# Kernel optimization log

Hardware: AMD Instinct MI355X
Metric: run time of the kernel (lower is better)

The kernel has to match this reference:

```python
import jax, jax.numpy as jnp
import numpy as np

EPS = 1e-6
NUM_CHANNELS = 8


def rotate_half(x):
    h = x.shape[-1] // 2
    return jnp.concatenate([-x[..., h:], x[..., :h]], axis=-1)


def l1_normalize(x):
    # torch F.normalize(p=1): x / max(||x||_1, eps) along last dim
    n = jnp.sum(jnp.abs(x), axis=-1, keepdims=True)
    return x / jnp.maximum(n, EPS)


def squared_softmax(x):      # potential_func_z = 'square'
    return l1_normalize(x * x)


def abs_normalization(x):    # potential_func_g = 'abs'
    return l1_normalize(jax.nn.relu(x))


def head_selection(qz, u, v, cos, sin):
    b, s, d = qz.shape
    C = NUM_CHANNELS
    r = u.shape[0] // C
    cos_e = cos[:, None]  # [b,1,s,r] (unsqueeze_dim=1)
    sin_e = sin[:, None]
    ap = lambda x: x * cos_e + rotate_half(x) * sin_e
    ap_o = lambda x: x * cos_e - rotate_half(x) * sin_e
    # [b,s,C*r] -> [b,C,s,r]
    qz_u = (qz @ u.T).reshape(b, s, C, r).transpose(0, 2, 1, 3)
    qz_v = (qz @ v.T).reshape(b, s, C, r).transpose(0, 2, 1, 3)
    qz_uo = ap_o(qz_u)
    qz_u = ap(qz_u)
    qz_v = ap(qz_v)
    msg_F = jnp.einsum('bcqr,bckr->bcqk', qz_u, qz_v)          # [b,C,s,s]
    # regularize_h = 1/dim_z -> softmax(F * dim_z)
    qh = jax.nn.softmax(msg_F.astype(jnp.float32) * d, axis=-1).astype(qz_u.dtype)
    qh_v1 = jnp.einsum('bcqk,bckr->bcqr', qh, qz_v)
    qh_v2 = jnp.einsum('bcqk,bcqr->bckr', qh, qz_uo)           # qh^T @ qz_uo
    qh_v1 = ap_o(qh_v1).transpose(0, 2, 1, 3).reshape(b, s, C * r)
    qh_v2 = ap(qh_v2).transpose(0, 2, 1, 3).reshape(b, s, C * r)
    return qh_v1 @ u + qh_v2 @ v                               # ternary_factor_scaling = 1


def topic_modeling(qz, w):
    qg = abs_normalization(qz @ w.T)     # binary_factor_scaling = regularize_g = 1
    return qg @ w


def period_message(qz, period_mat, period_attn):
    # info = P @ qz @ A, single term since _lambda = 0
    return jnp.einsum('qk,bkd->bqd', period_mat, qz) @ period_attn


def reference(unary, cos, sin, ternary_u, ternary_v, binary_factor,
              period_mat, period_attn, num_iters):
    # mean-field iterator: qz = act_z((unary + messages)/regularize_z), regularize_z = 1
    qz = squared_softmax(unary)
    for _ in range(num_iters):
        msg = (head_selection(qz, ternary_u, ternary_v, cos, sin)
               + topic_modeling(qz, binary_factor)
               + period_message(qz, period_mat, period_attn))
        qz = squared_softmax(unary + msg)
    return qz


def setup_inputs() -> dict:
    key = jax.random.key(0)
    ks = jax.random.split(key, 4)
    b, s, d, dff = 2, 2048, 256, 1024
    C = NUM_CHANNELS
    r = d // C  # head_dim = 32
    unary = jax.random.normal(ks[0], (b, s, d), dtype=jnp.float32)
    # RoPE tables (theta = 10000)
    inv_freq = 1.0 / (10000.0 ** (np.arange(0, r, 2, dtype=np.float32) / r))
    pos = np.arange(s, dtype=np.float32)
    freqs = pos[:, None] * inv_freq[None, :]
    emb = np.concatenate([freqs, freqs], axis=-1)               # [s, r]
    cos = jnp.broadcast_to(jnp.asarray(np.cos(emb))[None], (b, s, r)).astype(jnp.float32)
    sin = jnp.broadcast_to(jnp.asarray(np.sin(emb))[None], (b, s, r)).astype(jnp.float32)
    std = 0.2
    ternary_u = jax.random.normal(ks[1], (C * r, d), dtype=jnp.float32) * std
    ternary_v = jax.random.normal(ks[2], (C * r, d), dtype=jnp.float32) * std
    binary_factor = jax.random.normal(ks[3], (dff, d), dtype=jnp.float32) * std
    # PTPeriod buffers: band |i-j| == 24, and decaying matrix (k=1 -> identity)
    i = np.arange(s)
    period_mat = jnp.asarray((np.abs(i[:, None] - i[None, :]) == 24).astype(np.float32))
    j = np.arange(d)
    dist = np.abs(j[:, None] - j[None, :]).astype(np.float32)
    attn = np.exp(-0.5 * dist ** 2)
    attn[dist >= 1.0] = 0.0
    period_attn = jnp.asarray(attn, dtype=jnp.float32)
    return {"unary": unary, "cos": cos, "sin": sin,
            "ternary_u": ternary_u, "ternary_v": ternary_v,
            "binary_factor": binary_factor,
            "period_mat": period_mat, "period_attn": period_attn,
            "num_iters": 3}
```

## Files before the change

### kernel.cpp

```cpp
#include <hip/hip_runtime.h>
#include <math.h>

#define B 2
#define S 2048
#define D 256
#define DFF 1024
#define NC 8
#define R 32
#define NITER 3
#define EPSV 1e-6f
#define MROW (B * S)
#define NSPLIT 4

typedef unsigned short u16;
typedef unsigned int u32;
typedef __attribute__((ext_vector_type(8))) short short8_t;
typedef __attribute__((ext_vector_type(4))) float f32x4;

#define MFMA16(a, b, c) __builtin_amdgcn_mfma_f32_16x16x32_bf16(a, b, c, 0, 0, 0)

__device__ inline u16 bf16_rne(float x) {
  u32 u = __float_as_uint(x);
  u32 r = u + 0x7FFFu + ((u >> 16) & 1u);
  return (u16)(r >> 16);
}
__device__ inline void split2(float x, u16& h, u16& l) {
  h = bf16_rne(x);
  float hf = __uint_as_float(((u32)h) << 16);
  l = bf16_rne(x - hf);
}
__device__ inline short8_t ld8(const u16* p) { return *(const short8_t*)p; }

__device__ inline u32 pk2(float a, float b) {
  u32 r;
  asm("v_cvt_pk_bf16_f32 %0, %1, %2" : "=v"(r) : "v"(a), "v"(b));
  return r;
}
__device__ inline short8_t pack8(float c0, float c1, float c2, float c3,
                                 float c4, float c5, float c6, float c7) {
  union { u32 w[4]; short8_t v; } u_;
  u_.w[0] = pk2(c0, c1);
  u_.w[1] = pk2(c2, c3);
  u_.w[2] = pk2(c4, c5);
  u_.w[3] = pk2(c6, c7);
  return u_.v;
}

__device__ inline void gload_lds16(const u16* g, u16* l) {
  __builtin_amdgcn_global_load_lds(
      (const __attribute__((address_space(1))) unsigned int*)g,
      (__attribute__((address_space(3))) unsigned int*)l, 16, 0, 0);
}

__global__ __launch_bounds__(256) void k_sqsm(const float* __restrict__ unary,
                                              const float* __restrict__ msgs,
                                              const float* __restrict__ qzp,
                                              const int* __restrict__ pcols,
                                              const float* __restrict__ pvals,
                                              const int* __restrict__ pcnt,
                                              float* __restrict__ outf,
                                              u16* __restrict__ qzz) {
  int row = blockIdx.x;
  int t = threadIdx.x;
  int i = row * D + t;
  float x = unary[i];
  if (msgs) {
    const size_t NEl = (size_t)MROW * D;
#pragma unroll
    for (int p = 0; p < NSPLIT; p++) x += msgs[p * NEl + i];
    int b = row >> 11, q = row & 2047;
    int n = pcnt[q];
    for (int j = 0; j < n; j++)
      x = fmaf(pvals[q * 16 + j], qzp[(size_t)(b * S + pcols[q * 16 + j]) * D + t], x);
  }
  float v = x * x;
  float s = v;
#pragma unroll
  for (int off = 32; off; off >>= 1) s += __shfl_down(s, off, 64);
  __shared__ float red[4];
  if ((t & 63) == 0) red[t >> 6] = s;
  __syncthreads();
  float tot = fmaxf(red[0] + red[1] + red[2] + red[3], EPSV);
  float y = v / tot;
  if (outf) outf[i] = y;
  u16 h, l;
  split2(y, h, l);
  size_t rb = (size_t)row * 512;
  qzz[rb + t] = h;
  qzz[rb + 256 + t] = l;
}

__global__ __launch_bounds__(256) void k_gemm_z(
    const u16* __restrict__ Az, const u16* __restrict__ Bz,
    int K2, int Kpart, int N,
    float* __restrict__ outbase,
    float* __restrict__ quv, float* __restrict__ qg, float* __restrict__ qzp) {
  int Kh = K2 / 3;
  int Alda = Kh * 2;
  int m0 = blockIdx.x * 128, n0 = blockIdx.y * 128;
  int kbeg = blockIdx.z * Kpart, kend = kbeg + Kpart;
  int tid = threadIdx.x;
  int wid = tid >> 6, lane = tid & 63;
  int lr = lane & 15, lg = lane >> 4;
  int wm = (wid >> 1) * 64, wn = (wid & 1) * 64;

  __shared__ alignas(16) u16 As[8192];
  __shared__ alignas(16) u16 Bs[8192];

  f32x4 acc[4][4];
#pragma unroll
  for (int fr = 0; fr < 4; fr++)
#pragma unroll
    for (int fc = 0; fc < 4; fc++) acc[fr][fc] = (f32x4){0.f, 0.f, 0.f, 0.f};

  for (int kk = kbeg; kk < kend; kk += 64) {
    int zsrc = (kk >= Kh) ? kk - Kh : kk;
    __syncthreads();
#pragma unroll
    for (int it = 0; it < 4; it++) {
      int f = (it * 256 + tid) * 16;
      int row = f >> 7;
      int c16 = ((f >> 4) & 7) ^ (row & 7);
      u16* ldst = (u16*)As + it * 2048 + wid * 512;
      gload_lds16(Az + (size_t)(m0 + row) * Alda + zsrc + c16 * 8, ldst);
      u16* ldstB = (u16*)Bs + it * 2048 + wid * 512;
      gload_lds16(Bz + (size_t)(n0 + row) * K2 + kk + c16 * 8, ldstB);
    }
    __syncthreads();
#pragma unroll
    for (int ks = 0; ks < 2; ks++) {
      int cb = ks * 4 + lg;
      int sw = (cb ^ (lr & 7)) << 3;
      short8_t af[4], bf[4];
#pragma unroll
      for (int fr = 0; fr < 4; fr++)
        af[fr] = *(const short8_t*)(As + ((wm + fr * 16 + lr) << 6) + sw);
#pragma unroll
      for (int fc = 0; fc < 4; fc++)
        bf[fc] = *(const short8_t*)(Bs + ((wn + fc * 16 + lr) << 6) + sw);
      __builtin_amdgcn_s_setprio(1);
#pragma unroll
      for (int fr = 0; fr < 4; fr++)
#pragma unroll
        for (int fc = 0; fc < 4; fc++)
          acc[fr][fc] = MFMA16(af[fr], bf[fc], acc[fr][fc]);
      __builtin_amdgcn_s_setprio(0);
    }
  }

  if (qg) {
#pragma unroll
    for (int fr = 0; fr < 4; fr++)
#pragma unroll
      for (int fc = 0; fc < 4; fc++)
#pragma unroll
        for (int i = 0; i < 4; i++) {
          int m = m0 + wm + fr * 16 + lg * 4 + i;
          int nn = n0 + wn + fc * 16 + lr;
          float x = acc[fr][fc][i];
          if (nn < 512) quv[(size_t)m * 512 + nn] = x;
          else if (nn < 1536) qg[(size_t)m * DFF + nn - 512] = fmaxf(x, 0.f);
          else qzp[(size_t)m * 256 + nn - 1536] = x;
        }
  } else {
    float* out = outbase + (size_t)blockIdx.z * ((size_t)gridDim.x * 128) * N;
#pragma unroll
    for (int fr = 0; fr < 4; fr++)
#pragma unroll
      for (int fc = 0; fc < 4; fc++)
#pragma unroll
        for (int i = 0; i < 4; i++) {
          int m = m0 + wm + fr * 16 + lg * 4 + i;
          int nn = n0 + wn + fc * 16 + lr;
          out[(size_t)m * N + nn] = acc[fr][fc][i];
        }
  }
}

__global__ __launch_bounds__(256) void k_rope_pre(
    const float* __restrict__ quv, const float* __restrict__ cosb,
    const float* __restrict__ sinb,
    u16* __restrict__ Ah, u16* __restrict__ Al,
    u16* __restrict__ Bvh, u16* __restrict__ Bvl,
    u16* __restrict__ BvTph, u16* __restrict__ AoTph) {
  int row = blockIdx.x;
  int b = row >> 11, s_ = row & 2047;
  int t = threadIdx.x, c = t >> 5, rr = t & 31;
  float qu = quv[(size_t)row * 512 + t];
  float qv = quv[(size_t)row * 512 + 256 + t];
  float ou = __shfl_xor(qu, 16, 64);
  float ov = __shfl_xor(qv, 16, 64);
  float ru = (rr < 16) ? -ou : ou;
  float rv = (rr < 16) ? -ov : ov;
  float cs = cosb[(size_t)(b * S + s_) * R + rr];
  float sn = sinb[(size_t)(b * S + s_) * R + rr];
  float a = (qu * cs + ru * sn) * 256.f;
  float ao = qu * cs - ru * sn;
  float bv = qv * cs + rv * sn;
  size_t o = ((size_t)(b * NC + c) * S + s_) * R + rr;
  int off = s_ & 63;
  int kt = off >> 4;
  int pp = (kt >> 1) * 32 + ((off >> 2) & 3) * 8 + (kt & 1) * 4 + (off & 3);
  size_t otp = ((size_t)(b * NC + c) * R + rr) * S + (size_t)((s_ & ~63) + pp);
  u16 h, l;
  split2(a, h, l);  Ah[o] = h;  Al[o] = l;
  split2(bv, h, l); Bvh[o] = h; Bvl[o] = l; BvTph[otp] = h;
  split2(ao, h, l); AoTph[otp] = h;
}

__global__ __launch_bounds__(1024) void k_attn1_mfma(
    const u16* __restrict__ Ah, const u16* __restrict__ Al,
    const u16* __restrict__ Bvh, const u16* __restrict__ Bvl,
    const u16* __restrict__ BvTph,
    float* __restrict__ O1, float* __restrict__ mbuf, float* __restrict__ lbuf) {
  int bidx = blockIdx.x;
  int xcd = bidx & 7, wv = bidx >> 3;
  int bc = xcd * 2 + (wv & 1);
  int tile = wv >> 1;
  int tid = threadIdx.x;
  int lane = tid & 63;
  int lr = lane & 15, lg = lane >> 4;
  int khs = tid >> 9;
  int w8 = (tid >> 6) & 7;
  int qr = tile * 128 + w8 * 16;
  const size_t ofs = (size_t)bc * S * R;
  const size_t ofsT = (size_t)bc * R * S;

  __shared__ alignas(16) u16 BvhS[2][2][2048];
  __shared__ alignas(16) u16 BvlS[2][2][2048];
  __shared__ alignas(16) u16 PvS[2][2][2048];
  __shared__ float cm_o[8][16][34];
  __shared__ float cm_m[8][16], cm_l[8][16];

  short8_t a_hi = ld8(Ah + ofs + (size_t)(qr + lr) * R + lg * 8);
  short8_t a_lo = ld8(Al + ofs + (size_t)(qr + lr) * R + lg * 8);

  f32x4 o0 = {0, 0, 0, 0}, o1 = {0, 0, 0, 0};
  float m_q = -1e30f, l_p = 0.f;

  int ci = (w8 & 3) * 64 + lane;
  int wql = (w8 & 3) * 512;

#define A1_STAGE(STEP, DB)                                                         \
  {                                                                                \
    int kb_ = khs * 1024 + (STEP) * 64;                                            \
    if (w8 < 4) {                                                                  \
      gload_lds16(Bvh + ofs + (size_t)(kb_ + (ci >> 2)) * R + (ci & 3) * 8,        \
                  &BvhS[DB][khs][wql]);                                            \
      gload_lds16(BvTph + ofsT + (size_t)(ci >> 3) * S + kb_ + (ci & 7) * 8,       \
                  &PvS[DB][khs][wql]);                                             \
    } else {                                                                       \
      gload_lds16(Bvl + ofs + (size_t)(kb_ + (ci >> 2)) * R + (ci & 3) * 8,        \
                  &BvlS[DB][khs][wql]);                                            \
    }                                                                              \
  }

  A1_STAGE(0, 0);
  for (int step = 0; step < 16; step++) {
    int db = step & 1;
    __syncthreads();
    if (step + 1 < 16) A1_STAGE(step + 1, db ^ 1);

    short8_t sbH[4], sbL[4], pvb[4];
#pragma unroll
    for (int kt = 0; kt < 4; kt++) {
      int ro = (kt * 16 + lr) * 32 + lg * 8;
      sbH[kt] = ld8(&BvhS[db][khs][ro]);
      sbL[kt] = ld8(&BvlS[db][khs][ro]);
    }
#pragma unroll
    for (int j = 0; j < 4; j++)
      pvb[j] = ld8(&PvS[db][khs][((j & 1) * 16 + lr) * 64 + (j >> 1) * 32 + lg * 8]);

    f32x4 c[4];
    __builtin_amdgcn_s_setprio(1);
#pragma unroll
    for (int kt = 0; kt < 4; kt++) {
      f32x4 cc = {0.f, 0.f, 0.f, 0.f};
      cc = MFMA16(sbH[kt], a_hi, cc);
      cc = MFMA16(sbH[kt], a_lo, cc);
      cc = MFMA16(sbL[kt], a_hi, cc);
      c[kt] = cc;
    }
    __builtin_amdgcn_s_setprio(0);
    float mx = -1e30f;
#pragma unroll
    for (int kt = 0; kt < 4; kt++)
#pragma unroll
      for (int i = 0; i < 4; i++) mx = fmaxf(mx, c[kt][i]);
    if (!__all((int)(mx <= m_q + 8.f))) {
      mx = fmaxf(mx, __shfl_xor(mx, 16, 64));
      mx = fmaxf(mx, __shfl_xor(mx, 32, 64));
      float mnew = fmaxf(m_q, mx);
      float sc = __expf(m_q - mnew);
      m_q = mnew;
      l_p *= sc;
#pragma unroll
      for (int i = 0; i < 4; i++) {
        float s4 = __shfl(sc, (lane & 48) | (lg * 4 + i), 64);
        o0[i] *= s4;
        o1[i] *= s4;
      }
    }
    float ps = 0.f;
#pragma unroll
    for (int kt = 0; kt < 4; kt++)
#pragma unroll
      for (int i = 0; i < 4; i++) {
        c[kt][i] = __expf(c[kt][i] - m_q);
        ps += c[kt][i];
      }
    l_p += ps;
    __builtin_amdgcn_s_setprio(1);
    short8_t f0h = pack8(c[0][0], c[0][1], c[0][2], c[0][3],
                         c[1][0], c[1][1], c[1][2], c[1][3]);
    short8_t f1h = pack8(c[2][0], c[2][1], c[2][2], c[2][3],
                         c[3][0], c[3][1], c[3][2], c[3][3]);
    o0 = MFMA16(f0h, pvb[0], o0);
    o1 = MFMA16(f0h, pvb[1], o1);
    o0 = MFMA16(f1h, pvb[2], o0);
    o1 = MFMA16(f1h, pvb[3], o1);
    __builtin_amdgcn_s_setprio(0);
  }

  float lq = l_p;
  lq += __shfl_xor(lq, 16, 64);
  lq += __shfl_xor(lq, 32, 64);
  float m4[4], l4[4];
#pragma unroll
  for (int i = 0; i < 4; i++) {
    int src = (lane & 48) | (lg * 4 + i);
    m4[i] = __shfl(m_q, src, 64);
    l4[i] = __shfl(lq, src, 64);
  }
  __syncthreads();
  if (khs == 1) {
#pragma unroll
    for (int i = 0; i < 4; i++) {
      int r_ = lg * 4 + i;
      cm_o[w8][r_][lr] = o0[i];
      cm_o[w8][r_][lr + 16] = o1[i];
      if (lr == 0) { cm_m[w8][r_] = m4[i]; cm_l[w8][r_] = l4[i]; }
    }
  }
  __syncthreads();
  if (khs == 0) {
#pragma unroll
    for (int i = 0; i < 4; i++) {
      int r_ = lg * 4 + i;
      int q = qr + r_;
      float mb = cm_m[w8][r_], lb = cm_l[w8][r_];
      float mN = fmaxf(m4[i], mb);
      float ea = __expf(m4[i] - mN), eb = __expf(mb - mN);
      float inv = 1.f / (l4[i] * ea + lb * eb);
      O1[ofs + (size_t)q * R + lr] = (o0[i] * ea + cm_o[w8][r_][lr] * eb) * inv;
      O1[ofs + (size_t)q * R + 16 + lr] = (o1[i] * ea + cm_o[w8][r_][lr + 16] * eb) * inv;
      if (lr == 0) {
        mbuf[(size_t)bc * S + q] = mN;
        lbuf[(size_t)bc * S + q] = inv;
      }
    }
  }
}

__global__ __launch_bounds__(1024) void k_attn2_mfma(
    const u16* __restrict__ Ah, const u16* __restrict__ Al,
    const u16* __restrict__ Bvh, const u16* __restrict__ Bvl,
    const u16* __restrict__ AoTph,
    const float* __restrict__ mbuf, const float* __restrict__ lbuf,
    float* __restrict__ O2) {
  int bidx = blockIdx.x;
  int xcd = bidx & 7, wv = bidx >> 3;
  int bc = xcd * 2 + (wv & 1);
  int tile = wv >> 1;
  int tid = threadIdx.x;
  int lane = tid & 63;
  int lr = lane & 15, lg = lane >> 4;
  int qhs = tid >> 9;
  int w8 = (tid >> 6) & 7;
  int kr = tile * 128 + w8 * 16;
  const size_t ofs = (size_t)bc * S * R;
  const size_t ofsT = (size_t)bc * R * S;

  __shared__ alignas(16) u16 AhS[2][2][2048];
  __shared__ alignas(16) u16 AlS[2][2][2048];
  __shared__ alignas(16) u16 PvS[2][2][2048];
  __shared__ float cm[8][16][34];

  short8_t bv_hi = ld8(Bvh + ofs + (size_t)(kr + lr) * R + lg * 8);
  short8_t bv_lo = ld8(Bvl + ofs + (size_t)(kr + lr) * R + lg * 8);

  f32x4 o0 = {0, 0, 0, 0}, o1 = {0, 0, 0, 0};

  int ci = (w8 & 3) * 64 + lane;
  int wql = (w8 & 3) * 512;

#define A2_STAGE(STEP, DB)                                                         \
  {                                                                                \
    int qb_ = qhs * 1024 + (STEP) * 64;                                            \
    if (w8 < 4) {                                                                  \
      gload_lds16(Ah + ofs + (size_t)(qb_ + (ci >> 2)) * R + (ci & 3) * 8,         \
                  &AhS[DB][qhs][wql]);                                             \
      gload_lds16(AoTph + ofsT + (size_t)(ci >> 3) * S + qb_ + (ci & 7) * 8,       \
                  &PvS[DB][qhs][wql]);                                             \
    } else {                                                                       \
      gload_lds16(Al + ofs + (size_t)(qb_ + (ci >> 2)) * R + (ci & 3) * 8,         \
                  &AlS[DB][qhs][wql]);                                             \
    }                                                                              \
  }

  A2_STAGE(0, 0);
  for (int step = 0; step < 16; step++) {
    int db = step & 1;
    __syncthreads();
    if (step + 1 < 16) A2_STAGE(step + 1, db ^ 1);

    short8_t saH[4], saL[4], pvb[4];
#pragma unroll
    for (int qt = 0; qt < 4; qt++) {
      int ro = (qt * 16 + lr) * 32 + lg * 8;
      saH[qt] = ld8(&AhS[db][qhs][ro]);
      saL[qt] = ld8(&AlS[db][qhs][ro]);
    }
#pragma unroll
    for (int j = 0; j < 4; j++)
      pvb[j] = ld8(&PvS[db][qhs][((j & 1) * 16 + lr) * 64 + (j >> 1) * 32 + lg * 8]);

    f32x4 c[4];
    __builtin_amdgcn_s_setprio(1);
#pragma unroll
    for (int qt = 0; qt < 4; qt++) {
      f32x4 cc = {0.f, 0.f, 0.f, 0.f};
      cc = MFMA16(saH[qt], bv_hi, cc);
      cc = MFMA16(saH[qt], bv_lo, cc);
      cc = MFMA16(saL[qt], bv_hi, cc);
      c[qt] = cc;
    }
    __builtin_amdgcn_s_setprio(0);
    size_t qa = (size_t)bc * S + qhs * 1024 + step * 64;
    float4 mq0 = *(const float4*)(mbuf + qa + lg * 4);
    float4 mq1 = *(const float4*)(mbuf + qa + 16 + lg * 4);
    float4 mq2 = *(const float4*)(mbuf + qa + 32 + lg * 4);
    float4 mq3 = *(const float4*)(mbuf + qa + 48 + lg * 4);
    float4 il0 = *(const float4*)(lbuf + qa + lg * 4);
    float4 il1 = *(const float4*)(lbuf + qa + 16 + lg * 4);
    float4 il2 = *(const float4*)(lbuf + qa + 32 + lg * 4);
    float4 il3 = *(const float4*)(lbuf + qa + 48 + lg * 4);
    c[0][0] = __expf(c[0][0] - mq0.x) * il0.x;
    c[0][1] = __expf(c[0][1] - mq0.y) * il0.y;
    c[0][2] = __expf(c[0][2] - mq0.z) * il0.z;
    c[0][3] = __expf(c[0][3] - mq0.w) * il0.w;
    c[1][0] = __expf(c[1][0] - mq1.x) * il1.x;
    c[1][1] = __expf(c[1][1] - mq1.y) * il1.y;
    c[1][2] = __expf(c[1][2] - mq1.z) * il1.z;
    c[1][3] = __expf(c[1][3] - mq1.w) * il1.w;
    c[2][0] = __expf(c[2][0] - mq2.x) * il2.x;
    c[2][1] = __expf(c[2][1] - mq2.y) * il2.y;
    c[2][2] = __expf(c[2][2] - mq2.z) * il2.z;
    c[2][3] = __expf(c[2][3] - mq2.w) * il2.w;
    c[3][0] = __expf(c[3][0] - mq3.x) * il3.x;
    c[3][1] = __expf(c[3][1] - mq3.y) * il3.y;
    c[3][2] = __expf(c[3][2] - mq3.z) * il3.z;
    c[3][3] = __expf(c[3][3] - mq3.w) * il3.w;
    __builtin_amdgcn_s_setprio(1);
    short8_t f0h = pack8(c[0][0], c[0][1], c[0][2], c[0][3],
                         c[1][0], c[1][1], c[1][2], c[1][3]);
    short8_t f1h = pack8(c[2][0], c[2][1], c[2][2], c[2][3],
                         c[3][0], c[3][1], c[3][2], c[3][3]);
    o0 = MFMA16(f0h, pvb[0], o0);
    o1 = MFMA16(f0h, pvb[1], o1);
    o0 = MFMA16(f1h, pvb[2], o0);
    o1 = MFMA16(f1h, pvb[3], o1);
    __builtin_amdgcn_s_setprio(0);
  }

  __syncthreads();
  if (qhs == 1) {
#pragma unroll
    for (int i = 0; i < 4; i++) {
      int r_ = lg * 4 + i;
      cm[w8][r_][lr] = o0[i];
      cm[w8][r_][lr + 16] = o1[i];
    }
  }
  __syncthreads();
  if (qhs == 0) {
#pragma unroll
    for (int i = 0; i < 4; i++) {
      int r_ = lg * 4 + i;
      int k = kr + r_;
      O2[ofs + (size_t)k * R + lr] = o0[i] + cm[w8][r_][lr];
      O2[ofs + (size_t)k * R + 16 + lr] = o1[i] + cm[w8][r_][lr + 16];
    }
  }
}

__global__ __launch_bounds__(256) void k_post(const float* __restrict__ O1,
                                              const float* __restrict__ O2,
                                              const float* __restrict__ cosb,
                                              const float* __restrict__ sinb,
                                              const float* __restrict__ qg,
                                              u16* __restrict__ Abz) {
  int row = blockIdx.x;
  int b = row >> 11, s_ = row & 2047;
  int t = threadIdx.x, c = t >> 5, rr = t & 31;
  size_t base = ((size_t)(b * NC + c) * S + s_) * R;
  float x1 = O1[base + rr], x2 = O2[base + rr];
  float o1 = O1[base + (rr ^ 16)], o2 = O2[base + (rr ^ 16)];
  float r1 = (rr < 16) ? -o1 : o1;
  float r2 = (rr < 16) ? -o2 : o2;
  float cs = cosb[(size_t)(b * S + s_) * R + rr];
  float sn = sinb[(size_t)(b * S + s_) * R + rr];
  float v1 = x1 * cs - r1 * sn;
  float v2 = x2 * cs + r2 * sn;
  size_t rb = (size_t)row * 3072;
  u16 h, l;
  split2(v1, h, l);
  Abz[rb + t] = h;        Abz[rb + 1536 + t] = l;
  split2(v2, h, l);
  Abz[rb + 256 + t] = h;  Abz[rb + 1792 + t] = l;
  float vq[4];
  float s = 0.f;
#pragma unroll
  for (int j = 0; j < 4; j++) {
    vq[j] = qg[(size_t)row * DFF + t + 256 * j];
    s += vq[j];
  }
#pragma unroll
  for (int off = 32; off; off >>= 1) s += __shfl_down(s, off, 64);
  __shared__ float red[4];
  if ((t & 63) == 0) red[t >> 6] = s;
  __syncthreads();
  float inv = 1.f / fmaxf(red[0] + red[1] + red[2] + red[3], EPSV);
#pragma unroll
  for (int j = 0; j < 4; j++) {
    split2(vq[j] * inv, h, l);
    Abz[rb + 512 + t + 256 * j] = h;
    Abz[rb + 2048 + t + 256 * j] = l;
  }
}

__global__ __launch_bounds__(256) void k_prep_bt(const float* __restrict__ u,
                                                 const float* __restrict__ v,
                                                 const float* __restrict__ w,
                                                 const float* __restrict__ pa,
                                                 u16* __restrict__ btz) {
  int n = blockIdx.x;
  int k = threadIdx.x;
  float val = (n < 256)    ? u[(size_t)n * 256 + k]
            : (n < 512)    ? v[(size_t)(n - 256) * 256 + k]
            : (n < 1536)   ? w[(size_t)(n - 512) * 256 + k]
                           : pa[(size_t)k * 256 + (n - 1536)];
  u16 h, l;
  split2(val, h, l);
  size_t rb = (size_t)n * 768;
  btz[rb + k] = h;
  btz[rb + 256 + k] = l;
  btz[rb + 512 + k] = h;
}

__global__ __launch_bounds__(256) void k_prep_uvwT(const float* __restrict__ u,
                                                   const float* __restrict__ v,
                                                   const float* __restrict__ w,
                                                   u16* __restrict__ uvwTz) {
  int n = blockIdx.x;
  size_t rb = (size_t)n * 4608;
  for (int k = threadIdx.x; k < 1536; k += 256) {
    float val = (k < 256) ? u[(size_t)k * 256 + n]
              : (k < 512) ? v[(size_t)(k - 256) * 256 + n]
                          : w[(size_t)(k - 512) * 256 + n];
    u16 h, l;
    split2(val, h, l);
    uvwTz[rb + k] = h;
    uvwTz[rb + 1536 + k] = l;
    uvwTz[rb + 3072 + k] = h;
  }
}

__global__ __launch_bounds__(256) void k_pm_build(const float* __restrict__ pm,
                                                  int* __restrict__ cols,
                                                  float* __restrict__ vals,
                                                  int* __restrict__ cnt) {
  int q = blockIdx.x;
  int t = threadIdx.x;
  float v[8];
  int c = 0;
#pragma unroll
  for (int j = 0; j < 8; j++) {
    v[j] = pm[(size_t)q * S + t * 8 + j];
    c += (v[j] != 0.f) ? 1 : 0;
  }
  int lane = t & 63, w = t >> 6;
  int pc = c;
#pragma unroll
  for (int off = 1; off < 64; off <<= 1) {
    int o = __shfl_up(pc, off, 64);
    if (lane >= off) pc += o;
  }
  __shared__ int wsum[4];
  if (lane == 63) wsum[w] = pc;
  __syncthreads();
  int base = 0;
  for (int i = 0; i < w; i++) base += wsum[i];
  int idx = base + pc - c;
#pragma unroll
  for (int j = 0; j < 8; j++) {
    if (v[j] != 0.f) {
      if (idx < 16) {
        cols[q * 16 + idx] = t * 8 + j;
        vals[q * 16 + idx] = v[j];
      }
      idx++;
    }
  }
  if (t == 255) {
    int tot = base + pc;
    cnt[q] = tot > 16 ? 16 : tot;
  }
}

extern "C" void kernel_launch(void* const* d_in, const int* in_sizes, int n_in,
                              void* d_out, int out_size, void* d_ws, size_t ws_size,
                              hipStream_t stream) {
  const float* unary = (const float*)d_in[0];
  const float* cosb = (const float*)d_in[1];
  const float* sinb = (const float*)d_in[2];
  const float* u = (const float*)d_in[3];
  const float* v = (const float*)d_in[4];
  const float* w = (const float*)d_in[5];
  const float* pm = (const float*)d_in[6];
  const float* pa = (const float*)d_in[7];

  const size_t NE = (size_t)MROW * D;
  const size_t NB = (size_t)B * NC * S * R;

  float* fp = (float*)d_ws;
  float* msgs = fp;                fp += NSPLIT * NE;
  float* quv = fp;                 fp += 2 * NE;
  float* qg = fp;                  fp += 4 * NE;
  float* qzp = fp;                 fp += NE;
  float* mbuf = fp;                fp += B * NC * S;
  float* lbuf = fp;                fp += B * NC * S;
  float* pvals = fp;               fp += S * 16;
  int* pcols = (int*)fp;           fp += S * 16;
  int* pcnt = (int*)fp;            fp += S;
  float* O1 = quv;
  float* O2 = quv + NE;

  u16* bb = (u16*)fp;
  u16* qzz = bb;                   bb += (size_t)MROW * 512;
  u16* Abz = bb;                   bb += (size_t)MROW * 3072;
  u16* btz = bb;                   bb += (size_t)1792 * 768;
  u16* uvwTz = bb;                 bb += (size_t)256 * 4608;
  u16* Ah = bb;                    bb += NB;
  u16* Al = bb;                    bb += NB;
  u16* Bvh = bb;                   bb += NB;
  u16* Bvl = bb;                   bb += NB;
  u16* BvTph = bb;                 bb += NB;
  u16* AoTph = bb;                 bb += NB;

  k_pm_build<<<S, 256, 0, stream>>>(pm, pcols, pvals, pcnt);
  k_prep_bt<<<1792, 256, 0, stream>>>(u, v, w, pa, btz);
  k_prep_uvwT<<<256, 256, 0, stream>>>(u, v, w, uvwTz);

  k_sqsm<<<MROW, 256, 0, stream>>>(unary, nullptr, nullptr, nullptr, nullptr, nullptr,
                                   nullptr, qzz);

  for (int it = 0; it < NITER; ++it) {
    k_gemm_z<<<dim3(32, 14, 1), 256, 0, stream>>>(qzz, btz, 768, 768, 1792,
                                                  nullptr, quv, qg, qzp);
    k_rope_pre<<<MROW, 256, 0, stream>>>(quv, cosb, sinb, Ah, Al, Bvh, Bvl, BvTph, AoTph);
    k_attn1_mfma<<<256, 1024, 0, stream>>>(Ah, Al, Bvh, Bvl, BvTph, O1, mbuf, lbuf);
    k_attn2_mfma<<<256, 1024, 0, stream>>>(Ah, Al, Bvh, Bvl, AoTph, mbuf, lbuf, O2);
    k_post<<<MROW, 256, 0, stream>>>(O1, O2, cosb, sinb, qg, Abz);
    k_gemm_z<<<dim3(32, 2, NSPLIT), 256, 0, stream>>>(Abz, uvwTz, 4608, 4608 / NSPLIT, 256,
                                                      msgs, nullptr, nullptr, nullptr);
    k_sqsm<<<MROW, 256, 0, stream>>>(unary, msgs, qzp, pcols, pvals, pcnt,
                                     (it == NITER - 1) ? (float*)d_out : nullptr, qzz);
  }
}
```

Baseline: 451.2 us.

## Fuse RoPE preprocessing into GEMM epilogue and switch softmax to exp2

Removes the separate k_rope_pre kernel. The first GEMM epilogue now applies rotary embedding, the hi/lo bf16 split and the transposed writes directly from the accumulators, so the quv intermediate is no longer written to or read back from global memory. The Q-side scale now folds in log2(e), which lets the attention kernels use exp2f in place of __expf, with the rescale threshold adjusted to match. The epilogue becomes heavier, with scattered transposed stores and cos/sin loads per row, which may cost some GEMM efficiency.

Result: no change. 448.9 us (-0.5%).

```diff
diff --git a/kernel.cpp b/kernel.cpp
--- a/kernel.cpp
+++ b/kernel.cpp
@@ -11,6 +11,8 @@
 #define EPSV 1e-6f
 #define MROW (B * S)
 #define NSPLIT 4
+#define SC_LOG2 (256.f * 1.44269504088896f)
+#define THR2 11.5416f
 
 typedef unsigned short u16;
 typedef unsigned int u32;
@@ -94,7 +96,11 @@
     const u16* __restrict__ Az, const u16* __restrict__ Bz,
     int K2, int Kpart, int N,
     float* __restrict__ outbase,
-    float* __restrict__ quv, float* __restrict__ qg, float* __restrict__ qzp) {
+    float* __restrict__ qg, float* __restrict__ qzp,
+    const float* __restrict__ cosb, const float* __restrict__ sinb,
+    u16* __restrict__ Ah, u16* __restrict__ Al,
+    u16* __restrict__ Bvh, u16* __restrict__ Bvl,
+    u16* __restrict__ BvTph, u16* __restrict__ AoTph) {
   int Kh = K2 / 3;
   int Alda = Kh * 2;
   int m0 = blockIdx.x * 128, n0 = blockIdx.y * 128;
@@ -149,19 +155,55 @@
   }
 
   if (qg) {
+    int nnb = n0 + wn;
 #pragma unroll
     for (int fr = 0; fr < 4; fr++)
 #pragma unroll
-      for (int fc = 0; fc < 4; fc++)
-#pragma unroll
-        for (int i = 0; i < 4; i++) {
-          int m = m0 + wm + fr * 16 + lg * 4 + i;
-          int nn = n0 + wn + fc * 16 + lr;
-          float x = acc[fr][fc][i];
-          if (nn < 512) quv[(size_t)m * 512 + nn] = x;
-          else if (nn < 1536) qg[(size_t)m * DFF + nn - 512] = fmaxf(x, 0.f);
-          else qzp[(size_t)m * 256 + nn - 1536] = x;
+      for (int i = 0; i < 4; i++) {
+        int m = m0 + wm + fr * 16 + lg * 4 + i;
+        if (nnb < 512) {
+          int b = m >> 11, s_ = m & 2047;
+          int off = s_ & 63;
+          int kt = off >> 4;
+          int pp = (kt >> 1) * 32 + ((off >> 2) & 3) * 8 + (kt & 1) * 4 + (off & 3);
+          int sb = (s_ & ~63) + pp;
+          size_t csb = (size_t)(b * S + s_) * R;
+          float cs0 = cosb[csb + lr], sn0 = sinb[csb + lr];
+          float cs1 = cosb[csb + 16 + lr], sn1 = sinb[csb + 16 + lr];
+#pragma unroll
+          for (int fe = 0; fe < 4; fe += 2) {
+            float v0 = acc[fr][fe][i], v1 = acc[fr][fe + 1][i];
+            int nn_e = nnb + fe * 16 + lr;
+            int cch = (nn_e & 255) >> 5;
+            size_t o0 = ((size_t)(b * NC + cch) * S + s_) * R + lr;
+            size_t t0 = ((size_t)(b * NC + cch) * R + lr) * S + sb;
+            size_t t1 = ((size_t)(b * NC + cch) * R + 16 + lr) * S + sb;
+            float rot0 = -v1, rot1 = v0;
+            u16 h, l;
+            if (nn_e < 256) {
+              split2((v0 * cs0 + rot0 * sn0) * SC_LOG2, h, l);
+              Ah[o0] = h; Al[o0] = l;
+              split2((v1 * cs1 + rot1 * sn1) * SC_LOG2, h, l);
+              Ah[o0 + 16] = h; Al[o0 + 16] = l;
+              AoTph[t0] = bf16_rne(v0 * cs0 - rot0 * sn0);
+              AoTph[t1] = bf16_rne(v1 * cs1 - rot1 * sn1);
+            } else {
+              split2(v0 * cs0 + rot0 * sn0, h, l);
+              Bvh[o0] = h; Bvl[o0] = l; BvTph[t0] = h;
+              split2(v1 * cs1 + rot1 * sn1, h, l);
+              Bvh[o0 + 16] = h; Bvl[o0 + 16] = l; BvTph[t1] = h;
+            }
+          }
+        } else {
+#pragma unroll
+          for (int fc = 0; fc < 4; fc++) {
+            int nn = nnb + fc * 16 + lr;
+            float x = acc[fr][fc][i];
+            if (nn < 1536) qg[(size_t)m * DFF + nn - 512] = fmaxf(x, 0.f);
+            else qzp[(size_t)m * 256 + nn - 1536] = x;
+          }
         }
+      }
   } else {
     float* out = outbase + (size_t)blockIdx.z * ((size_t)gridDim.x * 128) * N;
 #pragma unroll
@@ -175,37 +217,6 @@
           out[(size_t)m * N + nn] = acc[fr][fc][i];
         }
   }
-}
-
-__global__ __launch_bounds__(256) void k_rope_pre(
-    const float* __restrict__ quv, const float* __restrict__ cosb,
-    const float* __restrict__ sinb,
-    u16* __restrict__ Ah, u16* __restrict__ Al,
-    u16* __restrict__ Bvh, u16* __restrict__ Bvl,
-    u16* __restrict__ BvTph, u16* __restrict__ AoTph) {
-  int row = blockIdx.x;
-  int b = row >> 11, s_ = row & 2047;
-  int t = threadIdx.x, c = t >> 5, rr = t & 31;
-  float qu = quv[(size_t)row * 512 + t];
-  float qv = quv[(size_t)row * 512 + 256 + t];
-  float ou = __shfl_xor(qu, 16, 64);
-  float ov = __shfl_xor(qv, 16, 64);
-  float ru = (rr < 16) ? -ou : ou;
-  float rv = (rr < 16) ? -ov : ov;
-  float cs = cosb[(size_t)(b * S + s_) * R + rr];
-  float sn = sinb[(size_t)(b * S + s_) * R + rr];
-  float a = (qu * cs + ru * sn) * 256.f;
-  float ao = qu * cs - ru * sn;
-  float bv = qv * cs + rv * sn;
-  size_t o = ((size_t)(b * NC + c) * S + s_) * R + rr;
-  int off = s_ & 63;
-  int kt = off >> 4;
-  int pp = (kt >> 1) * 32 + ((off >> 2) & 3) * 8 + (kt & 1) * 4 + (off & 3);
-  size_t otp = ((size_t)(b * NC + c) * R + rr) * S + (size_t)((s_ & ~63) + pp);
-  u16 h, l;
-  split2(a, h, l);  Ah[o] = h;  Al[o] = l;
-  split2(bv, h, l); Bvh[o] = h; Bvl[o] = l; BvTph[otp] = h;
-  split2(ao, h, l); AoTph[otp] = h;
 }
 
 __global__ __launch_bounds__(1024) void k_attn1_mfma(
@@ -288,11 +299,11 @@
     for (int kt = 0; kt < 4; kt++)
 #pragma unroll
       for (int i = 0; i < 4; i++) mx = fmaxf(mx, c[kt][i]);
-    if (!__all((int)(mx <= m_q + 8.f))) {
+    if (!__all((int)(mx <= m_q + THR2))) {
       mx = fmaxf(mx, __shfl_xor(mx, 16, 64));
       mx = fmaxf(mx, __shfl_xor(mx, 32, 64));
       float mnew = fmaxf(m_q, mx);
-      float sc = __expf(m_q - mnew);
+      float sc = exp2f(m_q - mnew);
       m_q = mnew;
       l_p *= sc;
 #pragma unroll
@@ -307,7 +318,7 @@
     for (int kt = 0; kt < 4; kt++)
 #pragma unroll
       for (int i = 0; i < 4; i++) {
-        c[kt][i] = __expf(c[kt][i] - m_q);
+        c[kt][i] = exp2f(c[kt][i] - m_q);
         ps += c[kt][i];
       }
     l_p += ps;
@@ -351,7 +362,7 @@
       int q = qr + r_;
       float mb = cm_m[w8][r_], lb = cm_l[w8][r_];
       float mN = fmaxf(m4[i], mb);
-      float ea = __expf(m4[i] - mN), eb = __expf(mb - mN);
+      float ea = exp2f(m4[i] - mN), eb = exp2f(mb - mN);
       float inv = 1.f / (l4[i] * ea + lb * eb);
       O1[ofs + (size_t)q * R + lr] = (o0[i] * ea + cm_o[w8][r_][lr] * eb) * inv;
       O1[ofs + (size_t)q * R + 16 + lr] = (o1[i] * ea + cm_o[w8][r_][lr + 16] * eb) * inv;
@@ -446,22 +457,22 @@
     float4 il1 = *(const float4*)(lbuf + qa + 16 + lg * 4);
     float4 il2 = *(const float4*)(lbuf + qa + 32 + lg * 4);
     float4 il3 = *(const float4*)(lbuf + qa + 48 + lg * 4);
-    c[0][0] = __expf(c[0][0] - mq0.x) * il0.x;
-    c[0][1] = __expf(c[0][1] - mq0.y) * il0.y;
-    c[0][2] = __expf(c[0][2] - mq0.z) * il0.z;
-    c[0][3] = __expf(c[0][3] - mq0.w) * il0.w;
-    c[1][0] = __expf(c[1][0] - mq1.x) * il1.x;
-    c[1][1] = __expf(c[1][1] - mq1.y) * il1.y;
-    c[1][2] = __expf(c[1][2] - mq1.z) * il1.z;
-    c[1][3] = __expf(c[1][3] - mq1.w) * il1.w;
-    c[2][0] = __expf(c[2][0] - mq2.x) * il2.x;
-    c[2][1] = __expf(c[2][1] - mq2.y) * il2.y;
-    c[2][2] = __expf(c[2][2] - mq2.z) * il2.z;
-    c[2][3] = __expf(c[2][3] - mq2.w) * il2.w;
-    c[3][0] = __expf(c[3][0] - mq3.x) * il3.x;
-    c[3][1] = __expf(c[3][1] - mq3.y) * il3.y;
-    c[3][2] = __expf(c[3][2] - mq3.z) * il3.z;
-    c[3][3] = __expf(c[3][3] - mq3.w) * il3.w;
+    c[0][0] = exp2f(c[0][0] - mq0.x) * il0.x;
+    c[0][1] = exp2f(c[0][1] - mq0.y) * il0.y;
+    c[0][2] = exp2f(c[0][2] - mq0.z) * il0.z;
+    c[0][3] = exp2f(c[0][3] - mq0.w) * il0.w;
+    c[1][0] = exp2f(c[1][0] - mq1.x) * il1.x;
+    c[1][1] = exp2f(c[1][1] - mq1.y) * il1.y;
+    c[1][2] = exp2f(c[1][2] - mq1.z) * il1.z;
+    c[1][3] = exp2f(c[1][3] - mq1.w) * il1.w;
+    c[2][0] = exp2f(c[2][0] - mq2.x) * il2.x;
+    c[2][1] = exp2f(c[2][1] - mq2.y) * il2.y;
+    c[2][2] = exp2f(c[2][2] - mq2.z) * il2.z;
+    c[2][3] = exp2f(c[2][3] - mq2.w) * il2.w;
+    c[3][0] = exp2f(c[3][0] - mq3.x) * il3.x;
+    c[3][1] = exp2f(c[3][1] - mq3.y) * il3.y;
+    c[3][2] = exp2f(c[3][2] - mq3.z) * il3.z;
+    c[3][3] = exp2f(c[3][3] - mq3.w) * il3.w;
     __builtin_amdgcn_s_setprio(1);
     short8_t f0h = pack8(c[0][0], c[0][1], c[0][2], c[0][3],
                          c[1][0], c[1][1], c[1][2], c[1][3]);
@@ -636,7 +647,8 @@
 
   float* fp = (float*)d_ws;
   float* msgs = fp;                fp += NSPLIT * NE;
-  float* quv = fp;                 fp += 2 * NE;
+  float* O1 = fp;                  fp += NE;
+  float* O2 = fp;                  fp += NE;
   float* qg = fp;                  fp += 4 * NE;
   float* qzp = fp;                 fp += NE;
   float* mbuf = fp;                fp += B * NC * S;
@@ -644,8 +656,6 @@
   float* pvals = fp;               fp += S * 16;
   int* pcols = (int*)fp;           fp += S * 16;
   int* pcnt = (int*)fp;            fp += S;
-  float* O1 = quv;
-  float* O2 = quv + NE;
 
   u16* bb = (u16*)fp;
   u16* qzz = bb;                   bb += (size_t)MROW * 512;
@@ -668,13 +678,15 @@
 
   for (int it = 0; it < NITER; ++it) {
     k_gemm_z<<<dim3(32, 14, 1), 256, 0, stream>>>(qzz, btz, 768, 768, 1792,
-                                                  nullptr, quv, qg, qzp);
-    k_rope_pre<<<MROW, 256, 0, stream>>>(quv, cosb, sinb, Ah, Al, Bvh, Bvl, BvTph, AoTph);
+                                                  nullptr, qg, qzp, cosb, sinb,
+                                                  Ah, Al, Bvh, Bvl, BvTph, AoTph);
     k_attn1_mfma<<<256, 1024, 0, stream>>>(Ah, Al, Bvh, Bvl, BvTph, O1, mbuf, lbuf);
     k_attn2_mfma<<<256, 1024, 0, stream>>>(Ah, Al, Bvh, Bvl, AoTph, mbuf, lbuf, O2);
     k_post<<<MROW, 256, 0, stream>>>(O1, O2, cosb, sinb, qg, Abz);
     k_gemm_z<<<dim3(32, 2, NSPLIT), 256, 0, stream>>>(Abz, uvwTz, 4608, 4608 / NSPLIT, 256,
-                                                      msgs, nullptr, nullptr, nullptr);
+                                                      msgs, nullptr, nullptr, nullptr, nullptr,
+                                                      nullptr, nullptr, nullptr, nullptr,
+                                                      nullptr, nullptr);
     k_sqsm<<<MROW, 256, 0, stream>>>(unary, msgs, qzp, pcols, pvals, pcnt,
                                      (it == NITER - 1) ? (float*)d_out : nullptr, qzz);
   }
```
